# Performance work log

Hardware: AMD Instinct MI355X
Metric: run time of the kernel (lower is better)

The kernel has to match this reference:

```python
import jax, jax.numpy as jnp
import numpy as np
from jax import lax

WIN = 9  # window size per spatial dim


def setup_inputs() -> dict:
    key = jax.random.key(0)
    k1, k2 = jax.random.split(key)
    shape = (2, 1, 160, 192, 160)  # [B, C=1, D, H, W]
    y_true = jax.random.uniform(k1, shape, dtype=jnp.float32)
    y_pred = jax.random.uniform(k2, shape, dtype=jnp.float32)
    return {"y_true": y_true, "y_pred": y_pred}


def reference(y_true, y_pred):
    Ii, Ji = y_true, y_pred
    ndims = Ii.ndim - 2  # 3 for volumes
    pad = WIN // 2
    # all five maps in the channel dim: [B, 5, D, H, W]
    all_five = jnp.concatenate([Ii, Ji, Ii * Ii, Ji * Ji, Ii * Ji], axis=1)
    # grouped box-filter conv: ones kernel [O=5, I/g=1, 9,9,9]
    kernel = jnp.ones((5, 1) + (WIN,) * ndims, dtype=Ii.dtype)
    conv = lax.conv_general_dilated(
        all_five, kernel,
        window_strides=(1,) * ndims,
        padding=[(pad, pad)] * ndims,
        feature_group_count=5,
        dimension_numbers=("NCDHW", "OIDHW", "NCDHW"),
    )
    I_sum, J_sum, I2_sum, J2_sum, IJ_sum = jnp.split(conv, 5, axis=1)
    win_size = jnp.asarray(float(WIN), dtype=Ii.dtype)
    cross = IJ_sum - J_sum / win_size * I_sum
    I_var = I2_sum - I_sum / win_size * I_sum
    J_var = J2_sum - J_sum / win_size * J_sum
    cc = cross * cross / (I_var * J_var + 1e-5)
    return -jnp.mean(cc)
```

## Files before the change

kernel.cpp:

```cpp
#include <hip/hip_runtime.h>

#define B_ 2
#define D_ 160
#define H_ 192
#define W_ 160
#define W4_ (W_ / 4)
#define HW_ (H_ * W_)
#define DHW_ (D_ * HW_)
#define NV_ ((long long)B_ * D_ * H_ * W_)

#define YH1 96
#define NYH (H_ / YH1)
#define SROWS (YH1 + 8)
#define SP 4
#define YCH1 12

#define ROWS2 8
#define ZCH2 10
#define NZC2 (D_ / ZCH2)
#define PAD 4
#define LROW (W_ + 2 * PAD)

#define A_YSTRIDE ((size_t)5 * W_)
#define A_ZSTRIDE ((size_t)5 * HW_)

typedef _Float16 half4 __attribute__((ext_vector_type(4)));

__global__ void k_zero(double* acc) { *acc = 0.0; }

__device__ __forceinline__ void add4h(float4& d, const half4 v) {
    d.x += (float)v.x; d.y += (float)v.y; d.z += (float)v.z; d.w += (float)v.w;
}
__device__ __forceinline__ void sub4h(float4& d, const half4 v) {
    d.x -= (float)v.x; d.y -= (float)v.y; d.z -= (float)v.z; d.w -= (float)v.w;
}

template<int SGN>
__device__ __forceinline__ void acc_lds(float4 s[5], const half4 ha, const half4 hb) {
    const float4 a = make_float4((float)ha.x, (float)ha.y, (float)ha.z, (float)ha.w);
    const float4 b = make_float4((float)hb.x, (float)hb.y, (float)hb.z, (float)hb.w);
    if (SGN > 0) {
        s[0].x += a.x;     s[0].y += a.y;     s[0].z += a.z;     s[0].w += a.w;
        s[1].x += b.x;     s[1].y += b.y;     s[1].z += b.z;     s[1].w += b.w;
        s[2].x += a.x*a.x; s[2].y += a.y*a.y; s[2].z += a.z*a.z; s[2].w += a.w*a.w;
        s[3].x += b.x*b.x; s[3].y += b.y*b.y; s[3].z += b.z*b.z; s[3].w += b.w*b.w;
        s[4].x += a.x*b.x; s[4].y += a.y*b.y; s[4].z += a.z*b.z; s[4].w += a.w*b.w;
    } else {
        s[0].x -= a.x;     s[0].y -= a.y;     s[0].z -= a.z;     s[0].w -= a.w;
        s[1].x -= b.x;     s[1].y -= b.y;     s[1].z -= b.z;     s[1].w -= b.w;
        s[2].x -= a.x*a.x; s[2].y -= a.y*a.y; s[2].z -= a.z*a.z; s[2].w -= a.w*a.w;
        s[3].x -= b.x*b.x; s[3].y -= b.y*b.y; s[3].z -= b.z*b.z; s[3].w -= b.w*b.w;
        s[4].x -= a.x*b.x; s[4].y -= a.y*b.y; s[4].z -= a.z*b.z; s[4].w -= a.w*b.w;
    }
}

__global__ __launch_bounds__(320) void k1_ysum(const float* __restrict__ I,
                                               const float* __restrict__ J,
                                               _Float16* __restrict__ A) {
    __shared__ _Float16 sI[SROWS][W_ + SP];
    __shared__ _Float16 sJ[SROWS][W_ + SP];
    const int tid = threadIdx.x;
    const int yh  = blockIdx.x % NYH;
    const int bz  = blockIdx.x / NYH;
    const int ylo = yh * YH1 - 4;

    const float* Ib = I + (size_t)bz * HW_;
    const float* Jb = J + (size_t)bz * HW_;

#pragma unroll
    for (int i = 0; i < 13; ++i) {
        const int idx = i * 320 + tid;
        const int lr  = idx / 40;
        const int g   = idx - lr * 40;
        const int gy  = ylo + lr;
        half4 hi, hj;
        hi.x = hi.y = hi.z = hi.w = (_Float16)0.f;
        hj.x = hj.y = hj.z = hj.w = (_Float16)0.f;
        if (gy >= 0 && gy < H_) {
            const float4 vi = *(const float4*)(Ib + (size_t)gy * W_ + g * 4);
            const float4 vj = *(const float4*)(Jb + (size_t)gy * W_ + g * 4);
            hi.x = (_Float16)vi.x; hi.y = (_Float16)vi.y; hi.z = (_Float16)vi.z; hi.w = (_Float16)vi.w;
            hj.x = (_Float16)vj.x; hj.y = (_Float16)vj.y; hj.z = (_Float16)vj.z; hj.w = (_Float16)vj.w;
        }
        *(half4*)&sI[lr][g * 4] = hi;
        *(half4*)&sJ[lr][g * 4] = hj;
    }
    __syncthreads();

    const int xg = tid % 40;
    const int yc = tid / 40;
    const int x4 = xg * 4;
    const int y0 = yh * YH1 + yc * YCH1;
    const int l0 = y0 - ylo;

    _Float16* Ap = A + (size_t)bz * A_ZSTRIDE + x4;

    float4 s[5];
#pragma unroll
    for (int c = 0; c < 5; ++c) s[c] = make_float4(0, 0, 0, 0);

#pragma unroll
    for (int j = 0; j < 8; ++j)
        acc_lds<+1>(s, *(const half4*)&sI[l0 - 4 + j][x4], *(const half4*)&sJ[l0 - 4 + j][x4]);

#pragma unroll
    for (int k = 0; k < YCH1; ++k) {
        const int ll = l0 + k + 4;
        acc_lds<+1>(s, *(const half4*)&sI[ll][x4], *(const half4*)&sJ[ll][x4]);
        if (k >= 1) {
            const int lt = l0 + k - 5;
            acc_lds<-1>(s, *(const half4*)&sI[lt][x4], *(const half4*)&sJ[lt][x4]);
        }
        _Float16* Ay = Ap + (size_t)(y0 + k) * A_YSTRIDE;
#pragma unroll
        for (int c = 0; c < 5; ++c) {
            half4 h;
            h.x = (_Float16)s[c].x; h.y = (_Float16)s[c].y;
            h.z = (_Float16)s[c].z; h.w = (_Float16)s[c].w;
            *(half4*)(Ay + c * W_) = h;
        }
    }
}

__global__ void k2_zxcc(const _Float16* __restrict__ A, double* __restrict__ acc) {
    __shared__ float sbuf[ROWS2][5][LROW];
    __shared__ float red[512];
    const int tid = threadIdx.x;
    const int r   = tid / W4_;
    const int l   = tid - r * W4_;
    const int x4  = l * 4;
    const int blk = blockIdx.x;
    const int zc  = blk % NZC2;
    const int rp  = blk / NZC2;
    const int gy  = rp * ROWS2 + r;
    const int b   = gy / H_;
    const int yy  = gy - b * H_;
    const int z0  = zc * ZCH2;

    {
        float* p = &sbuf[0][0][0];
        for (int i = tid; i < ROWS2 * 5 * LROW; i += ROWS2 * W4_) p[i] = 0.f;
    }

    const _Float16* Abase = A + (size_t)b * D_ * A_ZSTRIDE + (size_t)yy * A_YSTRIDE + x4;

    float4 s[5];
#pragma unroll
    for (int c = 0; c < 5; ++c) s[c] = make_float4(0, 0, 0, 0);
#pragma unroll
    for (int j = 0; j < 9; ++j) {
        const int zi = z0 - 5 + j;
        if (zi >= 0) {
            const _Float16* Az = Abase + (size_t)zi * A_ZSTRIDE;
#pragma unroll
            for (int c = 0; c < 5; ++c)
                add4h(s[c], *(const half4*)(Az + c * W_));
        }
    }
    __syncthreads();

    float local = 0.f;
    for (int k = 0; k < ZCH2; ++k) {
        const int zi = z0 + k + 4;
        if (zi < D_) {
            const _Float16* Az = Abase + (size_t)zi * A_ZSTRIDE;
#pragma unroll
            for (int c = 0; c < 5; ++c)
                add4h(s[c], *(const half4*)(Az + c * W_));
        }
        const int zo = z0 + k - 5;
        if (zo >= 0) {
            const _Float16* Az = Abase + (size_t)zo * A_ZSTRIDE;
#pragma unroll
            for (int c = 0; c < 5; ++c)
                sub4h(s[c], *(const half4*)(Az + c * W_));
        }
#pragma unroll
        for (int c = 0; c < 5; ++c)
            *(float4*)&sbuf[r][c][PAD + x4] = s[c];
        __syncthreads();

        float4 S5[5];
#pragma unroll
        for (int c = 0; c < 5; ++c) {
            const float4 a0 = *(const float4*)&sbuf[r][c][x4];
            const float4 a1 = *(const float4*)&sbuf[r][c][x4 + 4];
            const float4 a2 = *(const float4*)&sbuf[r][c][x4 + 8];
            const float o0 = a0.x + a0.y + a0.z + a0.w + a1.x + a1.y + a1.z + a1.w + a2.x;
            const float o1 = o0 - a0.x + a2.y;
            const float o2 = o1 - a0.y + a2.z;
            const float o3 = o2 - a0.z + a2.w;
            S5[c] = make_float4(o0, o1, o2, o3);
        }
        const float inv9 = 1.0f / 9.0f;
        {
            const float cr = S5[4].x - S5[1].x * S5[0].x * inv9;
            const float iv = S5[2].x - S5[0].x * S5[0].x * inv9;
            const float jv = S5[3].x - S5[1].x * S5[1].x * inv9;
            local += cr * cr / (iv * jv + 1e-5f);
        }
        {
            const float cr = S5[4].y - S5[1].y * S5[0].y * inv9;
            const float iv = S5[2].y - S5[0].y * S5[0].y * inv9;
            const float jv = S5[3].y - S5[1].y * S5[1].y * inv9;
            local += cr * cr / (iv * jv + 1e-5f);
        }
        {
            const float cr = S5[4].z - S5[1].z * S5[0].z * inv9;
            const float iv = S5[2].z - S5[0].z * S5[0].z * inv9;
            const float jv = S5[3].z - S5[1].z * S5[1].z * inv9;
            local += cr * cr / (iv * jv + 1e-5f);
        }
        {
            const float cr = S5[4].w - S5[1].w * S5[0].w * inv9;
            const float iv = S5[2].w - S5[0].w * S5[0].w * inv9;
            const float jv = S5[3].w - S5[1].w * S5[1].w * inv9;
            local += cr * cr / (iv * jv + 1e-5f);
        }
        __syncthreads();
    }

    red[tid] = local;
    if (tid < 192) red[320 + tid] = 0.f;
    __syncthreads();
    for (int off = 256; off > 0; off >>= 1) {
        if (tid < off) red[tid] += red[tid + off];
        __syncthreads();
    }
    if (tid == 0) atomicAdd(acc, (double)red[0]);
}

__global__ void p_direct(const float* __restrict__ I, const float* __restrict__ J,
                         double* __restrict__ acc) {
    const long long idx = (long long)blockIdx.x * blockDim.x + threadIdx.x;
    float local = 0.f;
    if (idx < NV_) {
        const int x = (int)(idx % W_);
        long long t = idx / W_;
        const int y = (int)(t % H_);
        t /= H_;
        const int z = (int)(t % D_);
        const int b = (int)(t / D_);
        const int z0 = max(z - 4, 0), z1 = min(z + 4, D_ - 1);
        const int y0 = max(y - 4, 0), y1 = min(y + 4, H_ - 1);
        const int x0 = max(x - 4, 0), x1 = min(x + 4, W_ - 1);
        float sI = 0.f, sJ = 0.f, sI2 = 0.f, sJ2 = 0.f, sIJ = 0.f;
        for (int zz = z0; zz <= z1; ++zz)
            for (int yy = y0; yy <= y1; ++yy) {
                const size_t row = ((size_t)(b * D_ + zz) * H_ + yy) * W_;
                for (int xx = x0; xx <= x1; ++xx) {
                    const float a = I[row + xx];
                    const float bb = J[row + xx];
                    sI += a; sJ += bb; sI2 += a * a; sJ2 += bb * bb; sIJ += a * bb;
                }
            }
        const float inv9 = 1.0f / 9.0f;
        const float cross = sIJ - sJ * sI * inv9;
        const float iv    = sI2 - sI * sI * inv9;
        const float jv    = sJ2 - sJ * sJ * inv9;
        local = cross * cross / (iv * jv + 1e-5f);
    }
    __shared__ float red[256];
    red[threadIdx.x] = local;
    __syncthreads();
    for (int off = 128; off > 0; off >>= 1) {
        if (threadIdx.x < off) red[threadIdx.x] += red[threadIdx.x + off];
        __syncthreads();
    }
    if (threadIdx.x == 0) atomicAdd(acc, (double)red[0]);
}

__global__ void k_final(const double* __restrict__ acc, float* __restrict__ out) {
    out[0] = (float)(-(*acc) / (double)NV_);
}

extern "C" void kernel_launch(void* const* d_in, const int* in_sizes, int n_in,
                              void* d_out, int out_size, void* d_ws, size_t ws_size,
                              hipStream_t stream) {
    const float* I = (const float*)d_in[0];
    const float* J = (const float*)d_in[1];
    float* out = (float*)d_out;

    const size_t needA = (size_t)5 * B_ * DHW_ * sizeof(_Float16);
    if (ws_size >= 1024 + needA) {
        double* acc = (double*)d_ws;
        _Float16* A = (_Float16*)((char*)d_ws + 1024);
        k_zero<<<1, 1, 0, stream>>>(acc);
        k1_ysum<<<B_ * D_ * NYH, 320, 0, stream>>>(I, J, A);
        k2_zxcc<<<NZC2 * (B_ * H_ / ROWS2), ROWS2 * W4_, 0, stream>>>(A, acc);
        k_final<<<1, 1, 0, stream>>>(acc, out);
    } else if (ws_size >= sizeof(double)) {
        double* acc = (double*)d_ws;
        k_zero<<<1, 1, 0, stream>>>(acc);
        p_direct<<<(int)((NV_ + 255) / 256), 256, 0, stream>>>(I, J, acc);
        k_final<<<1, 1, 0, stream>>>(acc, out);
    }
}
```

Measured before the change: 89.36 us.

## Software-pipeline z-slice loads in k2 and shrink k1 y-chunk size

The z-sum/cc kernel now double-buffers its half4 global loads in registers, issuing the next slice's add and subtract loads before processing the current slice. This is meant to hide global memory latency behind the LDS x-window and cc arithmetic, at the cost of more live registers. Out-of-range indices are clamped so loads are always issued and are then ignored by predication. The y-sum kernel halves its rows per block and per thread, which doubles the block count for more parallelism but adds relatively more halo rows.

New measurement: 212.5 us. 2.38x slower.

```diff
diff --git a/kernel.cpp b/kernel.cpp
--- a/kernel.cpp
+++ b/kernel.cpp
@@ -9,11 +9,11 @@
 #define DHW_ (D_ * HW_)
 #define NV_ ((long long)B_ * D_ * H_ * W_)
 
-#define YH1 96
+#define YH1 48
 #define NYH (H_ / YH1)
 #define SROWS (YH1 + 8)
-#define SP 4
-#define YCH1 12
+#define SSTRH (W_ + 4)
+#define YCH1 6
 
 #define ROWS2 8
 #define ZCH2 10
@@ -36,7 +36,7 @@
 }
 
 template<int SGN>
-__device__ __forceinline__ void acc_lds(float4 s[5], const half4 ha, const half4 hb) {
+__device__ __forceinline__ void accPr(float4 s[5], const half4 ha, const half4 hb) {
     const float4 a = make_float4((float)ha.x, (float)ha.y, (float)ha.z, (float)ha.w);
     const float4 b = make_float4((float)hb.x, (float)hb.y, (float)hb.z, (float)hb.w);
     if (SGN > 0) {
@@ -57,8 +57,8 @@
 __global__ __launch_bounds__(320) void k1_ysum(const float* __restrict__ I,
                                                const float* __restrict__ J,
                                                _Float16* __restrict__ A) {
-    __shared__ _Float16 sI[SROWS][W_ + SP];
-    __shared__ _Float16 sJ[SROWS][W_ + SP];
+    __shared__ _Float16 sI[SROWS][SSTRH];
+    __shared__ _Float16 sJ[SROWS][SSTRH];
     const int tid = threadIdx.x;
     const int yh  = blockIdx.x % NYH;
     const int bz  = blockIdx.x / NYH;
@@ -68,7 +68,7 @@
     const float* Jb = J + (size_t)bz * HW_;
 
 #pragma unroll
-    for (int i = 0; i < 13; ++i) {
+    for (int i = 0; i < 7; ++i) {
         const int idx = i * 320 + tid;
         const int lr  = idx / 40;
         const int g   = idx - lr * 40;
@@ -91,25 +91,25 @@
     const int yc = tid / 40;
     const int x4 = xg * 4;
     const int y0 = yh * YH1 + yc * YCH1;
-    const int l0 = y0 - ylo;
+    const int l0 = yc * YCH1 + 4;
 
     _Float16* Ap = A + (size_t)bz * A_ZSTRIDE + x4;
 
     float4 s[5];
 #pragma unroll
-    for (int c = 0; c < 5; ++c) s[c] = make_float4(0, 0, 0, 0);
+    for (int c = 0; c < 5; ++c) s[c] = make_float4(0.f, 0.f, 0.f, 0.f);
 
 #pragma unroll
     for (int j = 0; j < 8; ++j)
-        acc_lds<+1>(s, *(const half4*)&sI[l0 - 4 + j][x4], *(const half4*)&sJ[l0 - 4 + j][x4]);
+        accPr<+1>(s, *(const half4*)&sI[l0 - 4 + j][x4], *(const half4*)&sJ[l0 - 4 + j][x4]);
 
 #pragma unroll
     for (int k = 0; k < YCH1; ++k) {
         const int ll = l0 + k + 4;
-        acc_lds<+1>(s, *(const half4*)&sI[ll][x4], *(const half4*)&sJ[ll][x4]);
+        accPr<+1>(s, *(const half4*)&sI[ll][x4], *(const half4*)&sJ[ll][x4]);
         if (k >= 1) {
             const int lt = l0 + k - 5;
-            acc_lds<-1>(s, *(const half4*)&sI[lt][x4], *(const half4*)&sJ[lt][x4]);
+            accPr<-1>(s, *(const half4*)&sI[lt][x4], *(const half4*)&sJ[lt][x4]);
         }
         _Float16* Ay = Ap + (size_t)(y0 + k) * A_YSTRIDE;
 #pragma unroll
@@ -122,7 +122,85 @@
     }
 }
 
-__global__ void k2_zxcc(const _Float16* __restrict__ A, double* __restrict__ acc) {
+__device__ __forceinline__ float4 xwin(const float* rowp, int x4) {
+    const float4 a0 = *(const float4*)(rowp + x4);
+    const float4 a1 = *(const float4*)(rowp + x4 + 4);
+    const float4 a2 = *(const float4*)(rowp + x4 + 8);
+    const float o0 = a0.x + a0.y + a0.z + a0.w + a1.x + a1.y + a1.z + a1.w + a2.x;
+    const float o1 = o0 - a0.x + a2.y;
+    const float o2 = o1 - a0.y + a2.z;
+    const float o3 = o2 - a0.z + a2.w;
+    return make_float4(o0, o1, o2, o3);
+}
+
+__device__ __forceinline__ float cc4(const float4 S0, const float4 S1, const float4 S2,
+                                     const float4 S3, const float4 S4) {
+    const float inv9 = 1.0f / 9.0f;
+    float a = 0.f;
+    { const float cr = S4.x - S1.x * S0.x * inv9;
+      const float iv = S2.x - S0.x * S0.x * inv9;
+      const float jv = S3.x - S1.x * S1.x * inv9;
+      a += cr * cr / (iv * jv + 1e-5f); }
+    { const float cr = S4.y - S1.y * S0.y * inv9;
+      const float iv = S2.y - S0.y * S0.y * inv9;
+      const float jv = S3.y - S1.y * S1.y * inv9;
+      a += cr * cr / (iv * jv + 1e-5f); }
+    { const float cr = S4.z - S1.z * S0.z * inv9;
+      const float iv = S2.z - S0.z * S0.z * inv9;
+      const float jv = S3.z - S1.z * S1.z * inv9;
+      a += cr * cr / (iv * jv + 1e-5f); }
+    { const float cr = S4.w - S1.w * S0.w * inv9;
+      const float iv = S2.w - S0.w * S0.w * inv9;
+      const float jv = S3.w - S1.w * S1.w * inv9;
+      a += cr * cr / (iv * jv + 1e-5f); }
+    return a;
+}
+
+#define K2_ISSUE(K, P) do {                                                   \
+    int zi_ = z0 + (K) + 4; if (zi_ > D_ - 1) zi_ = D_ - 1;                   \
+    int zo_ = z0 + (K) - 5; if (zo_ < 0) zo_ = 0;                             \
+    const _Float16* pi_ = Abase + (size_t)zi_ * A_ZSTRIDE;                    \
+    const _Float16* po_ = Abase + (size_t)zo_ * A_ZSTRIDE;                    \
+    P##l0 = *(const half4*)(pi_ + 0 * W_);                                    \
+    P##l1 = *(const half4*)(pi_ + 1 * W_);                                    \
+    P##l2 = *(const half4*)(pi_ + 2 * W_);                                    \
+    P##l3 = *(const half4*)(pi_ + 3 * W_);                                    \
+    P##l4 = *(const half4*)(pi_ + 4 * W_);                                    \
+    P##t0 = *(const half4*)(po_ + 0 * W_);                                    \
+    P##t1 = *(const half4*)(po_ + 1 * W_);                                    \
+    P##t2 = *(const half4*)(po_ + 2 * W_);                                    \
+    P##t3 = *(const half4*)(po_ + 3 * W_);                                    \
+    P##t4 = *(const half4*)(po_ + 4 * W_);                                    \
+} while (0)
+
+#define K2_STEP(K, P) do {                                                    \
+    if (z0 + (K) + 4 < D_) {                                                  \
+        add4h(s0, P##l0); add4h(s1, P##l1); add4h(s2, P##l2);                 \
+        add4h(s3, P##l3); add4h(s4, P##l4);                                   \
+    }                                                                         \
+    if (z0 + (K) - 5 >= 0) {                                                  \
+        sub4h(s0, P##t0); sub4h(s1, P##t1); sub4h(s2, P##t2);                 \
+        sub4h(s3, P##t3); sub4h(s4, P##t4);                                   \
+    }                                                                         \
+    *(float4*)&sbuf[r][0][PAD + x4] = s0;                                     \
+    *(float4*)&sbuf[r][1][PAD + x4] = s1;                                     \
+    *(float4*)&sbuf[r][2][PAD + x4] = s2;                                     \
+    *(float4*)&sbuf[r][3][PAD + x4] = s3;                                     \
+    *(float4*)&sbuf[r][4][PAD + x4] = s4;                                     \
+    __syncthreads();                                                          \
+    {                                                                         \
+        const float4 S0_ = xwin(&sbuf[r][0][0], x4);                          \
+        const float4 S1_ = xwin(&sbuf[r][1][0], x4);                          \
+        const float4 S2_ = xwin(&sbuf[r][2][0], x4);                          \
+        const float4 S3_ = xwin(&sbuf[r][3][0], x4);                          \
+        const float4 S4_ = xwin(&sbuf[r][4][0], x4);                          \
+        local += cc4(S0_, S1_, S2_, S3_, S4_);                                \
+    }                                                                         \
+    __syncthreads();                                                          \
+} while (0)
+
+__global__ __launch_bounds__(320) void k2_zxcc(const _Float16* __restrict__ A,
+                                               double* __restrict__ acc) {
     __shared__ float sbuf[ROWS2][5][LROW];
     __shared__ float red[512];
     const int tid = threadIdx.x;
@@ -144,80 +222,33 @@
 
     const _Float16* Abase = A + (size_t)b * D_ * A_ZSTRIDE + (size_t)yy * A_YSTRIDE + x4;
 
-    float4 s[5];
-#pragma unroll
-    for (int c = 0; c < 5; ++c) s[c] = make_float4(0, 0, 0, 0);
+    float4 s0 = make_float4(0.f, 0.f, 0.f, 0.f);
+    float4 s1 = s0, s2 = s0, s3 = s0, s4 = s0;
 #pragma unroll
     for (int j = 0; j < 9; ++j) {
         const int zi = z0 - 5 + j;
         if (zi >= 0) {
             const _Float16* Az = Abase + (size_t)zi * A_ZSTRIDE;
-#pragma unroll
-            for (int c = 0; c < 5; ++c)
-                add4h(s[c], *(const half4*)(Az + c * W_));
+            add4h(s0, *(const half4*)(Az + 0 * W_));
+            add4h(s1, *(const half4*)(Az + 1 * W_));
+            add4h(s2, *(const half4*)(Az + 2 * W_));
+            add4h(s3, *(const half4*)(Az + 3 * W_));
+            add4h(s4, *(const half4*)(Az + 4 * W_));
         }
     }
     __syncthreads();
 
     float local = 0.f;
-    for (int k = 0; k < ZCH2; ++k) {
-        const int zi = z0 + k + 4;
-        if (zi < D_) {
-            const _Float16* Az = Abase + (size_t)zi * A_ZSTRIDE;
-#pragma unroll
-            for (int c = 0; c < 5; ++c)
-                add4h(s[c], *(const half4*)(Az + c * W_));
-        }
-        const int zo = z0 + k - 5;
-        if (zo >= 0) {
-            const _Float16* Az = Abase + (size_t)zo * A_ZSTRIDE;
-#pragma unroll
-            for (int c = 0; c < 5; ++c)
-                sub4h(s[c], *(const half4*)(Az + c * W_));
-        }
-#pragma unroll
-        for (int c = 0; c < 5; ++c)
-            *(float4*)&sbuf[r][c][PAD + x4] = s[c];
-        __syncthreads();
-
-        float4 S5[5];
-#pragma unroll
-        for (int c = 0; c < 5; ++c) {
-            const float4 a0 = *(const float4*)&sbuf[r][c][x4];
-            const float4 a1 = *(const float4*)&sbuf[r][c][x4 + 4];
-            const float4 a2 = *(const float4*)&sbuf[r][c][x4 + 8];
-            const float o0 = a0.x + a0.y + a0.z + a0.w + a1.x + a1.y + a1.z + a1.w + a2.x;
-            const float o1 = o0 - a0.x + a2.y;
-            const float o2 = o1 - a0.y + a2.z;
-            const float o3 = o2 - a0.z + a2.w;
-            S5[c] = make_float4(o0, o1, o2, o3);
-        }
-        const float inv9 = 1.0f / 9.0f;
-        {
-            const float cr = S5[4].x - S5[1].x * S5[0].x * inv9;
-            const float iv = S5[2].x - S5[0].x * S5[0].x * inv9;
-            const float jv = S5[3].x - S5[1].x * S5[1].x * inv9;
-            local += cr * cr / (iv * jv + 1e-5f);
-        }
-        {
-            const float cr = S5[4].y - S5[1].y * S5[0].y * inv9;
-            const float iv = S5[2].y - S5[0].y * S5[0].y * inv9;
-            const float jv = S5[3].y - S5[1].y * S5[1].y * inv9;
-            local += cr * cr / (iv * jv + 1e-5f);
-        }
-        {
-            const float cr = S5[4].z - S5[1].z * S5[0].z * inv9;
-            const float iv = S5[2].z - S5[0].z * S5[0].z * inv9;
-            const float jv = S5[3].z - S5[1].z * S5[1].z * inv9;
-            local += cr * cr / (iv * jv + 1e-5f);
-        }
-        {
-            const float cr = S5[4].w - S5[1].w * S5[0].w * inv9;
-            const float iv = S5[2].w - S5[0].w * S5[0].w * inv9;
-            const float jv = S5[3].w - S5[1].w * S5[1].w * inv9;
-            local += cr * cr / (iv * jv + 1e-5f);
-        }
-        __syncthreads();
+    half4 Al0, Al1, Al2, Al3, Al4, At0, At1, At2, At3, At4;
+    half4 Bl0, Bl1, Bl2, Bl3, Bl4, Bt0, Bt1, Bt2, Bt3, Bt4;
+
+    K2_ISSUE(0, A);
+#pragma unroll
+    for (int kk = 0; kk < ZCH2; kk += 2) {
+        K2_ISSUE(kk + 1, B);
+        K2_STEP(kk, A);
+        K2_ISSUE(kk + 2, A);
+        K2_STEP(kk + 1, B);
     }
 
     red[tid] = local;
```
